# Optimization experiments

Measured on AMD Instinct MI355X. Metric: run time of the kernel, lower is better.

The kernel has to match this reference:

```python
import math
import jax, jax.numpy as jnp
import numpy as np

TAU = 1.0
EPS = 1e-6


def _make_projection(m, d, seed=0):
    # FAVOR+ projection: stacked orthogonal d x d blocks (QR of gaussian),
    # rows rescaled by norms of gaussian rows (scaling=0 in the torch code).
    rng = np.random.default_rng(seed)
    blocks = []
    nb_full = m // d
    for _ in range(nb_full):
        q, _ = np.linalg.qr(rng.standard_normal((d, d)))
        blocks.append(q.T)
    rem = m - nb_full * d
    if rem > 0:
        q, _ = np.linalg.qr(rng.standard_normal((d, d)))
        blocks.append(q.T[:rem])
    mat = np.vstack(blocks)
    mult = np.linalg.norm(rng.standard_normal((m, d)), axis=1)
    return jnp.asarray((mult[:, None] * mat).astype(np.float32))


def setup_inputs() -> dict:
    B, N, H, D, d, m = 16, 4096, 8, 64, 64, 128
    key = jax.random.key(0)
    k1, k2, k3 = jax.random.split(key, 3)
    return {
        "x": jax.random.normal(k1, (B, N, H, D), jnp.float32),
        "node_vec1": jax.random.normal(k2, (B, N, H, d), jnp.float32),
        "node_vec2": jax.random.normal(k3, (B, N, H, d), jnp.float32),
        "proj": _make_projection(m, d),
    }


def _feature_map(data, proj, is_query):
    # data: [B,N,H,d], proj: [m,d]
    d = data.shape[-1]
    data = data * (1.0 / jnp.sqrt(jnp.sqrt(jnp.float32(d))))
    ratio = 1.0 / jnp.sqrt(jnp.float32(proj.shape[0]))
    data_dash = jnp.einsum('bnhd,md->bnhm', data, proj)
    diag = 0.5 * jnp.sum(data * data, axis=-1, keepdims=True)  # [B,N,H,1]
    if is_query:
        mx = jnp.max(data_dash, axis=-1, keepdims=True)
    else:
        # max over feature dim then over sequence/node dim (axis 1)
        mx = jnp.max(jnp.max(data_dash, axis=-1, keepdims=True), axis=1, keepdims=True)
    return ratio * (jnp.exp(data_dash - diag - mx) + EPS)


def reference(x, node_vec1, node_vec2, proj):
    inv_sqrt_tau = 1.0 / math.sqrt(TAU)
    v1p = _feature_map(node_vec1 * inv_sqrt_tau, proj, True)   # [B,N,H,m]
    v2p = _feature_map(node_vec2 * inv_sqrt_tau, proj, False)  # [B,N,H,m]
    # linear (kernelized) attention: O(N) in sequence length
    v2x = jnp.einsum('bnhm,bnhd->bhmd', v2p, x)                 # [B,H,m,D]
    out1 = jnp.einsum('bnhm,bhmd->bnhd', v1p, v2x)              # [B,N,H,D]
    v2_sum = jnp.sum(v2p, axis=1)                               # [B,H,m]
    out2 = jnp.einsum('bnhm,bhm->bnh', v1p, v2_sum)[..., None]  # [B,N,H,1]
    return (out1 / out2, v1p, v2p)
```

## Files before the change

kernel.cpp:

```cpp
#include <hip/hip_runtime.h>
#include <math.h>

constexpr int CN = 4096, CHH = 8, CD = 64, CM = 128;
constexpr int V1P_OFF = 16 * 4096 * 8 * 64;
constexpr int V2P_OFF = V1P_OFF + 16 * 4096 * 8 * 128;
constexpr float KSCALE = 0.35355339059327373f;
constexpr float KRATIO = 0.08838834764831843f;
constexpr float KEPS   = 1e-6f;

typedef __attribute__((ext_vector_type(8))) short bf16x8;
typedef __attribute__((ext_vector_type(4))) float f32x4;

__device__ __forceinline__ float dot4(float4 a, float4 b) {
  return fmaf(a.x, b.x, fmaf(a.y, b.y, fmaf(a.z, b.z, a.w * b.w)));
}
__device__ __forceinline__ float4 scl4(float4 a, float s) {
  return make_float4(a.x * s, a.y * s, a.z * s, a.w * s);
}
__device__ __forceinline__ short bhi(float f) {
  return (short)(__float_as_uint(f) >> 16);
}
__device__ __forceinline__ float bf2f(short s) {
  return __uint_as_float(((unsigned)(unsigned short)s) << 16);
}
__device__ __forceinline__ void split8(float4 u, float4 v, bf16x8& hi, bf16x8& lo) {
  float a[8] = {u.x, u.y, u.z, u.w, v.x, v.y, v.z, v.w};
#pragma unroll
  for (int e = 0; e < 8; e++) {
    short h = bhi(a[e]);
    hi[e] = h;
    lo[e] = bhi(a[e] - bf2f(h));
  }
}
__device__ __forceinline__ void split8a(const float* a, bf16x8& hi, bf16x8& lo) {
#pragma unroll
  for (int e = 0; e < 8; e++) {
    short h = bhi(a[e]);
    hi[e] = h;
    lo[e] = bhi(a[e] - bf2f(h));
  }
}

#define MFMA_B16(A, B, C) __builtin_amdgcn_mfma_f32_16x16x32_bf16(A, B, C, 0, 0, 0)

#define LOAD_BFRAGS(proj, lm, ko)                                   \
  bf16x8 Bh0[8], Bl0[8], Bh1[8], Bl1[8];                            \
  _Pragma("unroll")                                                 \
  for (int t = 0; t < 8; t++) {                                     \
    const float* pb = (proj) + (t * 16 + (lm)) * 64 + (ko);         \
    float4 p0 = *(const float4*)(pb);                               \
    float4 p1 = *(const float4*)(pb + 4);                           \
    float4 p2 = *(const float4*)(pb + 32);                          \
    float4 p3 = *(const float4*)(pb + 36);                          \
    split8(p0, p1, Bh0[t], Bl0[t]);                                 \
    split8(p2, p3, Bh1[t], Bl1[t]);                                 \
  }

#define PROJ_MFMA(acc, t)                                           \
  do {                                                              \
    acc = MFMA_B16(Ah0, Bh0[t], acc);                               \
    acc = MFMA_B16(Ah1, Bh1[t], acc);                               \
    acc = MFMA_B16(Al0, Bh0[t], acc);                               \
    acc = MFMA_B16(Al1, Bh1[t], acc);                               \
    acc = MFMA_B16(Ah0, Bl0[t], acc);                               \
    acc = MFMA_B16(Ah1, Bl1[t], acc);                               \
  } while (0)

__global__ __launch_bounds__(256) void kp_stat(
    const float* __restrict__ inp, const float* __restrict__ proj,
    float* __restrict__ outmax) {
  const int l = threadIdx.x & 63, w = threadIdx.x >> 6;
  const int lm = l & 15, lk = l >> 4, ko = lk * 8;
  LOAD_BFRAGS(proj, lm, ko);
  const int bh = blockIdx.x >> 3, ch = blockIdx.x & 7;
  const int b = bh >> 3, h = bh & 7;
  float bmax = -1e30f;
  for (int s = 0; s < 8; s++) {
    const int nb = ch * 512 + w * 128 + s * 16;
    const size_t rA = (size_t)((b * CN + nb + lm) * CHH + h);
    const float* pa = inp + rA * 64 + ko;
    float4 a0 = scl4(*(const float4*)(pa), KSCALE);
    float4 a1 = scl4(*(const float4*)(pa + 4), KSCALE);
    float4 a2 = scl4(*(const float4*)(pa + 32), KSCALE);
    float4 a3 = scl4(*(const float4*)(pa + 36), KSCALE);
    bf16x8 Ah0, Al0, Ah1, Al1;
    split8(a0, a1, Ah0, Al0);
    split8(a2, a3, Ah1, Al1);
    float rm[4] = {-1e30f, -1e30f, -1e30f, -1e30f};
#pragma unroll
    for (int t = 0; t < 8; t++) {
      f32x4 acc = {0.f, 0.f, 0.f, 0.f};
      PROJ_MFMA(acc, t);
#pragma unroll
      for (int r = 0; r < 4; r++) rm[r] = fmaxf(rm[r], acc[r]);
    }
    bmax = fmaxf(fmaxf(bmax, fmaxf(rm[0], rm[1])), fmaxf(rm[2], rm[3]));
  }
  float v = bmax;
#pragma unroll
  for (int d = 1; d < 64; d <<= 1) v = fmaxf(v, __shfl_xor(v, d));
  __shared__ float wred[4];
  if (l == 0) wred[w] = v;
  __syncthreads();
  if (threadIdx.x == 0)
    outmax[blockIdx.x] = fmaxf(fmaxf(wred[0], wred[1]), fmaxf(wred[2], wred[3]));
}

__global__ void k2b_max(const float* __restrict__ partmax, float* __restrict__ wmax) {
  const int bh = threadIdx.x;
  float m = -1e30f;
#pragma unroll
  for (int c = 0; c < 8; c++) m = fmaxf(m, partmax[bh * 8 + c]);
  wmax[bh] = m;
}

__global__ __launch_bounds__(256) void kp_emit(
    const float* __restrict__ inp, const float* __restrict__ proj,
    const float* __restrict__ mxin, float* __restrict__ outp) {
  const int l = threadIdx.x & 63, w = threadIdx.x >> 6;
  const int lm = l & 15, lk = l >> 4, ko = lk * 8;
  LOAD_BFRAGS(proj, lm, ko);
  const int bh = blockIdx.x >> 3, ch = blockIdx.x & 7;
  const int b = bh >> 3, h = bh & 7;
  const float whm = mxin[bh];
  for (int s = 0; s < 8; s++) {
    const int nb = ch * 512 + w * 128 + s * 16;
    const size_t rA = (size_t)((b * CN + nb + lm) * CHH + h);
    const float* pa = inp + rA * 64 + ko;
    float4 a0 = scl4(*(const float4*)(pa), KSCALE);
    float4 a1 = scl4(*(const float4*)(pa + 4), KSCALE);
    float4 a2 = scl4(*(const float4*)(pa + 32), KSCALE);
    float4 a3 = scl4(*(const float4*)(pa + 36), KSCALE);
    bf16x8 Ah0, Al0, Ah1, Al1;
    split8(a0, a1, Ah0, Al0);
    split8(a2, a3, Ah1, Al1);
    float dp = dot4(a0, a0) + dot4(a1, a1) + dot4(a2, a2) + dot4(a3, a3);
    dp += __shfl_xor(dp, 16);
    dp += __shfl_xor(dp, 32);
    float c[4];
    size_t obase[4];
#pragma unroll
    for (int r = 0; r < 4; r++) {
      const float dg = __shfl(dp, lk * 4 + r);
      const size_t rr = (size_t)((b * CN + nb + lk * 4 + r) * CHH + h);
      c[r] = -(0.5f * dg + whm);
      obase[r] = rr * CM + lm;
    }
#pragma unroll
    for (int t = 0; t < 8; t++) {
      f32x4 acc = {0.f, 0.f, 0.f, 0.f};
      PROJ_MFMA(acc, t);
#pragma unroll
      for (int r = 0; r < 4; r++)
        outp[obase[r] + t * 16] = KRATIO * (__expf(acc[r] + c[r]) + KEPS);
    }
  }
}

__global__ __launch_bounds__(256) void kv1e(
    const float* __restrict__ inp, const float* __restrict__ proj,
    float* __restrict__ outp) {
  const int l = threadIdx.x & 63, w = threadIdx.x >> 6;
  const int lm = l & 15, lk = l >> 4, ko = lk * 8;
  LOAD_BFRAGS(proj, lm, ko);
  const int bh = blockIdx.x >> 3, ch = blockIdx.x & 7;
  const int b = bh >> 3, h = bh & 7;
  for (int s = 0; s < 8; s++) {
    const int nb = ch * 512 + w * 128 + s * 16;
    const size_t rA = (size_t)((b * CN + nb + lm) * CHH + h);
    const float* pa = inp + rA * 64 + ko;
    float4 a0 = scl4(*(const float4*)(pa), KSCALE);
    float4 a1 = scl4(*(const float4*)(pa + 4), KSCALE);
    float4 a2 = scl4(*(const float4*)(pa + 32), KSCALE);
    float4 a3 = scl4(*(const float4*)(pa + 36), KSCALE);
    bf16x8 Ah0, Al0, Ah1, Al1;
    split8(a0, a1, Ah0, Al0);
    split8(a2, a3, Ah1, Al1);
    float dp = dot4(a0, a0) + dot4(a1, a1) + dot4(a2, a2) + dot4(a3, a3);
    dp += __shfl_xor(dp, 16);
    dp += __shfl_xor(dp, 32);
    f32x4 acc8[8];
#pragma unroll
    for (int t = 0; t < 8; t++) {
      f32x4 acc = {0.f, 0.f, 0.f, 0.f};
      PROJ_MFMA(acc, t);
      acc8[t] = acc;
    }
    float rm[4];
#pragma unroll
    for (int r = 0; r < 4; r++) {
      float m = acc8[0][r];
#pragma unroll
      for (int t = 1; t < 8; t++) m = fmaxf(m, acc8[t][r]);
      m = fmaxf(m, __shfl_xor(m, 1));
      m = fmaxf(m, __shfl_xor(m, 2));
      m = fmaxf(m, __shfl_xor(m, 4));
      m = fmaxf(m, __shfl_xor(m, 8));
      rm[r] = m;
    }
    float c[4];
    size_t obase[4];
#pragma unroll
    for (int r = 0; r < 4; r++) {
      const float dg = __shfl(dp, lk * 4 + r);
      const size_t rr = (size_t)((b * CN + nb + lk * 4 + r) * CHH + h);
      c[r] = -(0.5f * dg + rm[r]);
      obase[r] = rr * CM + lm;
    }
#pragma unroll
    for (int t = 0; t < 8; t++) {
#pragma unroll
      for (int r = 0; r < 4; r++)
        outp[obase[r] + t * 16] = KRATIO * (__expf(acc8[t][r] + c[r]) + KEPS);
    }
  }
}

__global__ __launch_bounds__(256) void k3m(
    const float* __restrict__ v2p, const float* __restrict__ x,
    float* __restrict__ part, float* __restrict__ vsumpart) {
  const int l = threadIdx.x & 63, w = threadIdx.x >> 6;
  const int lm = l & 15, lk = l >> 4;
  const int bh = blockIdx.x >> 3, ch = blockIdx.x & 7;
  const int b = bh >> 3, h = bh & 7;
  const int jt0 = w * 2;
  f32x4 acc[2][4];
#pragma unroll
  for (int jj = 0; jj < 2; jj++)
#pragma unroll
    for (int dt = 0; dt < 4; dt++) acc[jj][dt] = (f32x4){0.f, 0.f, 0.f, 0.f};
  float vs0 = 0.f, vs1 = 0.f;
  for (int t = 0; t < 16; t++) {
    const int n0 = ch * 512 + t * 32 + lk * 8;
    bf16x8 Ah[2], Al[2];
#pragma unroll
    for (int jj = 0; jj < 2; jj++) {
      float af[8];
#pragma unroll
      for (int e = 0; e < 8; e++)
        af[e] = v2p[(size_t)((b * CN + n0 + e) * CHH + h) * CM + (jt0 + jj) * 16 + lm];
      split8a(af, Ah[jj], Al[jj]);
      float p = 0.f;
#pragma unroll
      for (int e = 0; e < 8; e++) p += af[e];
      if (jj == 0) vs0 += p; else vs1 += p;
    }
#pragma unroll
    for (int dt = 0; dt < 4; dt++) {
      float bfv[8];
#pragma unroll
      for (int e = 0; e < 8; e++)
        bfv[e] = x[(size_t)((b * CN + n0 + e) * CHH + h) * CD + dt * 16 + lm];
      bf16x8 Bh, Bl;
      split8a(bfv, Bh, Bl);
#pragma unroll
      for (int jj = 0; jj < 2; jj++) {
        acc[jj][dt] = MFMA_B16(Ah[jj], Bh, acc[jj][dt]);
        acc[jj][dt] = MFMA_B16(Al[jj], Bh, acc[jj][dt]);
        acc[jj][dt] = MFMA_B16(Ah[jj], Bl, acc[jj][dt]);
      }
    }
  }
  const size_t pbase = (size_t)blockIdx.x * 8192;
#pragma unroll
  for (int jj = 0; jj < 2; jj++)
#pragma unroll
    for (int dt = 0; dt < 4; dt++)
#pragma unroll
      for (int r = 0; r < 4; r++)
        part[pbase + ((size_t)(jt0 + jj) * 16 + lk * 4 + r) * 64 + dt * 16 + lm] = acc[jj][dt][r];
  float v0 = vs0, v1 = vs1;
  v0 += __shfl_xor(v0, 16); v0 += __shfl_xor(v0, 32);
  v1 += __shfl_xor(v1, 16); v1 += __shfl_xor(v1, 32);
  if (lk == 0) {
    vsumpart[(size_t)blockIdx.x * 128 + (jt0 + 0) * 16 + lm] = v0;
    vsumpart[(size_t)blockIdx.x * 128 + (jt0 + 1) * 16 + lm] = v1;
  }
}

__global__ void k3b_reduce(const float* __restrict__ part, const float* __restrict__ vsumpart,
                           float* __restrict__ v2x, float* __restrict__ vsum) {
  const int i = blockIdx.x * 256 + threadIdx.x;
  if (i < 1048576) {
    const int bh = i >> 13, r = i & 8191;
    float s = 0.f;
#pragma unroll
    for (int c = 0; c < 8; c++) s += part[(size_t)(bh * 8 + c) * 8192 + r];
    v2x[i] = s;
  } else if (i < 1048576 + 16384) {
    const int k = i - 1048576, bh = k >> 7, j = k & 127;
    float s = 0.f;
#pragma unroll
    for (int c = 0; c < 8; c++) s += vsumpart[(size_t)(bh * 8 + c) * 128 + j];
    vsum[k] = s;
  }
}

__global__ __launch_bounds__(256) void k4m(
    const float* __restrict__ v1p, const float* __restrict__ v2xg,
    const float* __restrict__ vsumg, float* __restrict__ out0) {
  const int l = threadIdx.x & 63, dt = threadIdx.x >> 6;
  const int lm = l & 15, lk = l >> 4;
  const int bh = blockIdx.x >> 4, ch = blockIdx.x & 15;
  const int b = bh >> 3, h = bh & 7;
  bf16x8 Bh[4], Bl[4];
#pragma unroll
  for (int kc = 0; kc < 4; kc++) {
    float bfv[8];
#pragma unroll
    for (int e = 0; e < 8; e++)
      bfv[e] = v2xg[(size_t)bh * 8192 + (size_t)(kc * 32 + lk * 8 + e) * 64 + dt * 16 + lm];
    split8a(bfv, Bh[kc], Bl[kc]);
  }
  float vsr[4][8];
#pragma unroll
  for (int kc = 0; kc < 4; kc++)
#pragma unroll
    for (int e = 0; e < 8; e++)
      vsr[kc][e] = vsumg[bh * 128 + kc * 32 + lk * 8 + e];
  for (int s = 0; s < 16; s++) {
    const int nb = ch * 256 + s * 16;
    const float* pa = v1p + (size_t)((b * CN + nb + lm) * CHH + h) * CM;
    bf16x8 Ah[4], Al[4];
    float o2p = 0.f;
#pragma unroll
    for (int kc = 0; kc < 4; kc++) {
      float4 u = *(const float4*)(pa + kc * 32 + lk * 8);
      float4 v = *(const float4*)(pa + kc * 32 + lk * 8 + 4);
      split8(u, v, Ah[kc], Al[kc]);
      o2p += u.x * vsr[kc][0] + u.y * vsr[kc][1] + u.z * vsr[kc][2] + u.w * vsr[kc][3]
           + v.x * vsr[kc][4] + v.y * vsr[kc][5] + v.z * vsr[kc][6] + v.w * vsr[kc][7];
    }
    o2p += __shfl_xor(o2p, 16);
    o2p += __shfl_xor(o2p, 32);
    f32x4 acc = {0.f, 0.f, 0.f, 0.f};
#pragma unroll
    for (int kc = 0; kc < 4; kc++) {
      acc = MFMA_B16(Ah[kc], Bh[kc], acc);
      acc = MFMA_B16(Al[kc], Bh[kc], acc);
      acc = MFMA_B16(Ah[kc], Bl[kc], acc);
    }
#pragma unroll
    for (int r = 0; r < 4; r++) {
      const float inv = 1.0f / __shfl(o2p, lk * 4 + r);
      out0[(size_t)((b * CN + nb + lk * 4 + r) * CHH + h) * CD + dt * 16 + lm] = acc[r] * inv;
    }
  }
}

extern "C" void kernel_launch(void* const* d_in, const int* in_sizes, int n_in,
                              void* d_out, int out_size, void* d_ws, size_t ws_size,
                              hipStream_t stream) {
  (void)in_sizes; (void)n_in; (void)out_size; (void)ws_size;
  const float* x    = (const float*)d_in[0];
  const float* nv1  = (const float*)d_in[1];
  const float* nv2  = (const float*)d_in[2];
  const float* proj = (const float*)d_in[3];
  float* out  = (float*)d_out;
  float* out0 = out;
  float* v1p  = out + V1P_OFF;
  float* v2p  = out + V2P_OFF;

  float* part     = v1p;
  float* vsumpart = v1p + 8388608;
  float* ws      = (float*)d_ws;
  float* wmax    = ws;
  float* vsum    = ws + 128;
  float* v2x     = ws + 16512;
  float* partmax = ws + 16512 + 1048576;

  kp_stat   <<<dim3(1024), dim3(256), 0, stream>>>(nv2, proj, partmax);
  k2b_max   <<<dim3(1),    dim3(128), 0, stream>>>(partmax, wmax);
  kp_emit   <<<dim3(1024), dim3(256), 0, stream>>>(nv2, proj, wmax, v2p);
  k3m       <<<dim3(1024), dim3(256), 0, stream>>>(v2p, x, part, vsumpart);
  k3b_reduce<<<dim3(4160), dim3(256), 0, stream>>>(part, vsumpart, v2x, vsum);
  kv1e      <<<dim3(1024), dim3(256), 0, stream>>>(nv1, proj, v1p);
  k4m       <<<dim3(2048), dim3(256), 0, stream>>>(v1p, v2x, vsum, out0);
}
```

Baseline: 507.9 us.

## Fuse v2 feature emission with v2p^T x accumulation via shared-memory tile

Merges the v2 feature-map emit kernel with the v2p-times-x partial GEMM kernel. Each block computes a 64-row tile of v2p features, writes them to global memory and to an LDS tile, then reads them back from LDS as MFMA operands together with x, and accumulates the column sums in registers. This avoids re-reading the 256 MB v2p tensor from global memory and removes one launch. In exchange it uses about 33 KB of LDS per block and two barriers per iteration, which may lower occupancy and serialise the exp and MFMA phases.

```diff
diff --git a/kernel.cpp b/kernel.cpp
--- a/kernel.cpp
+++ b/kernel.cpp
@@ -114,19 +114,30 @@
   wmax[bh] = m;
 }
 
-__global__ __launch_bounds__(256) void kp_emit(
-    const float* __restrict__ inp, const float* __restrict__ proj,
-    const float* __restrict__ mxin, float* __restrict__ outp) {
+__global__ __launch_bounds__(256) void kemit3(
+    const float* __restrict__ nv2, const float* __restrict__ x,
+    const float* __restrict__ proj, const float* __restrict__ mxin,
+    float* __restrict__ v2p, float* __restrict__ part,
+    float* __restrict__ vsumpart) {
+  __shared__ float tile[64 * 129];
+  __shared__ float vred[4][128];
   const int l = threadIdx.x & 63, w = threadIdx.x >> 6;
   const int lm = l & 15, lk = l >> 4, ko = lk * 8;
   LOAD_BFRAGS(proj, lm, ko);
   const int bh = blockIdx.x >> 3, ch = blockIdx.x & 7;
   const int b = bh >> 3, h = bh & 7;
   const float whm = mxin[bh];
+  const int jt0 = w * 2;
+  f32x4 acc[2][4];
+#pragma unroll
+  for (int jj = 0; jj < 2; jj++)
+#pragma unroll
+    for (int dt = 0; dt < 4; dt++) acc[jj][dt] = (f32x4){0.f, 0.f, 0.f, 0.f};
+  float vs[8] = {0.f, 0.f, 0.f, 0.f, 0.f, 0.f, 0.f, 0.f};
   for (int s = 0; s < 8; s++) {
-    const int nb = ch * 512 + w * 128 + s * 16;
+    const int nb = ch * 512 + s * 64 + w * 16;
     const size_t rA = (size_t)((b * CN + nb + lm) * CHH + h);
-    const float* pa = inp + rA * 64 + ko;
+    const float* pa = nv2 + rA * 64 + ko;
     float4 a0 = scl4(*(const float4*)(pa), KSCALE);
     float4 a1 = scl4(*(const float4*)(pa + 4), KSCALE);
     float4 a2 = scl4(*(const float4*)(pa + 32), KSCALE);
@@ -148,12 +159,67 @@
     }
 #pragma unroll
     for (int t = 0; t < 8; t++) {
-      f32x4 acc = {0.f, 0.f, 0.f, 0.f};
-      PROJ_MFMA(acc, t);
+      f32x4 a = {0.f, 0.f, 0.f, 0.f};
+      PROJ_MFMA(a, t);
+#pragma unroll
+      for (int r = 0; r < 4; r++) {
+        const float val = KRATIO * (__expf(a[r] + c[r]) + KEPS);
+        v2p[obase[r] + t * 16] = val;
+        tile[(w * 16 + lk * 4 + r) * 129 + t * 16 + lm] = val;
+        vs[t] += val;
+      }
+    }
+    __syncthreads();
+#pragma unroll
+    for (int ks = 0; ks < 2; ks++) {
+      bf16x8 Ah[2], Al[2];
+#pragma unroll
+      for (int jj = 0; jj < 2; jj++) {
+        float af[8];
+#pragma unroll
+        for (int e = 0; e < 8; e++)
+          af[e] = tile[(ks * 32 + lk * 8 + e) * 129 + (jt0 + jj) * 16 + lm];
+        split8a(af, Ah[jj], Al[jj]);
+      }
+      const int n0 = ch * 512 + s * 64 + ks * 32 + lk * 8;
+#pragma unroll
+      for (int dt = 0; dt < 4; dt++) {
+        float bfv[8];
+#pragma unroll
+        for (int e = 0; e < 8; e++)
+          bfv[e] = x[(size_t)((b * CN + n0 + e) * CHH + h) * CD + dt * 16 + lm];
+        bf16x8 Bh, Bl;
+        split8a(bfv, Bh, Bl);
+#pragma unroll
+        for (int jj = 0; jj < 2; jj++) {
+          acc[jj][dt] = MFMA_B16(Ah[jj], Bh, acc[jj][dt]);
+          acc[jj][dt] = MFMA_B16(Al[jj], Bh, acc[jj][dt]);
+          acc[jj][dt] = MFMA_B16(Ah[jj], Bl, acc[jj][dt]);
+        }
+      }
+    }
+    __syncthreads();
+  }
+  const size_t pbase = (size_t)blockIdx.x * 8192;
+#pragma unroll
+  for (int jj = 0; jj < 2; jj++)
+#pragma unroll
+    for (int dt = 0; dt < 4; dt++)
 #pragma unroll
       for (int r = 0; r < 4; r++)
-        outp[obase[r] + t * 16] = KRATIO * (__expf(acc[r] + c[r]) + KEPS);
-    }
+        part[pbase + ((size_t)(jt0 + jj) * 16 + lk * 4 + r) * 64 + dt * 16 + lm] = acc[jj][dt][r];
+#pragma unroll
+  for (int t = 0; t < 8; t++) {
+    float v = vs[t];
+    v += __shfl_xor(v, 16);
+    v += __shfl_xor(v, 32);
+    if (lk == 0) vred[w][t * 16 + lm] = v;
+  }
+  __syncthreads();
+  if (threadIdx.x < 128) {
+    const int j = threadIdx.x;
+    vsumpart[(size_t)blockIdx.x * 128 + j] =
+        vred[0][j] + vred[1][j] + vred[2][j] + vred[3][j];
   }
 }
 
@@ -216,68 +282,6 @@
   }
 }
 
-__global__ __launch_bounds__(256) void k3m(
-    const float* __restrict__ v2p, const float* __restrict__ x,
-    float* __restrict__ part, float* __restrict__ vsumpart) {
-  const int l = threadIdx.x & 63, w = threadIdx.x >> 6;
-  const int lm = l & 15, lk = l >> 4;
-  const int bh = blockIdx.x >> 3, ch = blockIdx.x & 7;
-  const int b = bh >> 3, h = bh & 7;
-  const int jt0 = w * 2;
-  f32x4 acc[2][4];
-#pragma unroll
-  for (int jj = 0; jj < 2; jj++)
-#pragma unroll
-    for (int dt = 0; dt < 4; dt++) acc[jj][dt] = (f32x4){0.f, 0.f, 0.f, 0.f};
-  float vs0 = 0.f, vs1 = 0.f;
-  for (int t = 0; t < 16; t++) {
-    const int n0 = ch * 512 + t * 32 + lk * 8;
-    bf16x8 Ah[2], Al[2];
-#pragma unroll
-    for (int jj = 0; jj < 2; jj++) {
-      float af[8];
-#pragma unroll
-      for (int e = 0; e < 8; e++)
-        af[e] = v2p[(size_t)((b * CN + n0 + e) * CHH + h) * CM + (jt0 + jj) * 16 + lm];
-      split8a(af, Ah[jj], Al[jj]);
-      float p = 0.f;
-#pragma unroll
-      for (int e = 0; e < 8; e++) p += af[e];
-      if (jj == 0) vs0 += p; else vs1 += p;
-    }
-#pragma unroll
-    for (int dt = 0; dt < 4; dt++) {
-      float bfv[8];
-#pragma unroll
-      for (int e = 0; e < 8; e++)
-        bfv[e] = x[(size_t)((b * CN + n0 + e) * CHH + h) * CD + dt * 16 + lm];
-      bf16x8 Bh, Bl;
-      split8a(bfv, Bh, Bl);
-#pragma unroll
-      for (int jj = 0; jj < 2; jj++) {
-        acc[jj][dt] = MFMA_B16(Ah[jj], Bh, acc[jj][dt]);
-        acc[jj][dt] = MFMA_B16(Al[jj], Bh, acc[jj][dt]);
-        acc[jj][dt] = MFMA_B16(Ah[jj], Bl, acc[jj][dt]);
-      }
-    }
-  }
-  const size_t pbase = (size_t)blockIdx.x * 8192;
-#pragma unroll
-  for (int jj = 0; jj < 2; jj++)
-#pragma unroll
-    for (int dt = 0; dt < 4; dt++)
-#pragma unroll
-      for (int r = 0; r < 4; r++)
-        part[pbase + ((size_t)(jt0 + jj) * 16 + lk * 4 + r) * 64 + dt * 16 + lm] = acc[jj][dt][r];
-  float v0 = vs0, v1 = vs1;
-  v0 += __shfl_xor(v0, 16); v0 += __shfl_xor(v0, 32);
-  v1 += __shfl_xor(v1, 16); v1 += __shfl_xor(v1, 32);
-  if (lk == 0) {
-    vsumpart[(size_t)blockIdx.x * 128 + (jt0 + 0) * 16 + lm] = v0;
-    vsumpart[(size_t)blockIdx.x * 128 + (jt0 + 1) * 16 + lm] = v1;
-  }
-}
-
 __global__ void k3b_reduce(const float* __restrict__ part, const float* __restrict__ vsumpart,
                            float* __restrict__ v2x, float* __restrict__ vsum) {
   const int i = blockIdx.x * 256 + threadIdx.x;
@@ -371,8 +375,7 @@
 
   kp_stat   <<<dim3(1024), dim3(256), 0, stream>>>(nv2, proj, partmax);
   k2b_max   <<<dim3(1),    dim3(128), 0, stream>>>(partmax, wmax);
-  kp_emit   <<<dim3(1024), dim3(256), 0, stream>>>(nv2, proj, wmax, v2p);
-  k3m       <<<dim3(1024), dim3(256), 0, stream>>>(v2p, x, part, vsumpart);
+  kemit3    <<<dim3(1024), dim3(256), 0, stream>>>(nv2, x, proj, wmax, v2p, part, vsumpart);
   k3b_reduce<<<dim3(4160), dim3(256), 0, stream>>>(part, vsumpart, v2x, vsum);
   kv1e      <<<dim3(1024), dim3(256), 0, stream>>>(nv1, proj, v1p);
   k4m       <<<dim3(2048), dim3(256), 0, stream>>>(v1p, v2x, vsum, out0);
```

Result: slower. 569.5 us (+12.1%).
